# Optimization experiments

Hardware: AMD Instinct MI355X
Metric: run time of the kernel (lower is better)

Reference implementation:

```python
import jax, jax.numpy as jnp
import numpy as np

B, S, D, H, FF = 2, 2048, 1024, 16, 4096
DK = D // H
EPS = 1e-5


def setup_inputs() -> dict:
    key = jax.random.key(0)
    ks = jax.random.split(key, 16)
    sd = 0.02
    return {
        "x": jax.random.normal(ks[0], (B, S, D), jnp.float32),
        "mask": jnp.ones((B, 1, 1, S), jnp.int32),
        "wq_w": jax.random.normal(ks[1], (D, D), jnp.float32) * sd,
        "wq_b": jnp.zeros((D,), jnp.float32),
        "wk_w": jax.random.normal(ks[2], (D, D), jnp.float32) * sd,
        "wk_b": jnp.zeros((D,), jnp.float32),
        "wv_w": jax.random.normal(ks[3], (D, D), jnp.float32) * sd,
        "wv_b": jnp.zeros((D,), jnp.float32),
        "wo_w": jax.random.normal(ks[4], (D, D), jnp.float32) * sd,
        "wo_b": jnp.zeros((D,), jnp.float32),
        "ff1_w": jax.random.normal(ks[5], (FF, D), jnp.float32) * sd,
        "ff1_b": jnp.zeros((FF,), jnp.float32),
        "ff2_w": jax.random.normal(ks[6], (D, FF), jnp.float32) * sd,
        "ff2_b": jnp.zeros((D,), jnp.float32),
        "ln1_a": jnp.ones((D,), jnp.float32),
        "ln1_b": jnp.zeros((D,), jnp.float32),
        "ln2_a": jnp.ones((D,), jnp.float32),
        "ln2_b": jnp.zeros((D,), jnp.float32),
    }


def _layernorm(x, alpha, beta):
    # Matches torch module: std is unbiased (ddof=1), divides by (std + eps)
    mean = jnp.mean(x, -1, keepdims=True)
    std = jnp.std(x, -1, keepdims=True, ddof=1)
    return (x - mean) / (std + EPS) * alpha + beta


def _mha(x, mask, wq_w, wq_b, wk_w, wk_b, wv_w, wv_b, wo_w, wo_b):
    q = (x @ wq_w.T + wq_b).reshape(B, S, H, DK).transpose(0, 2, 1, 3)
    k = (x @ wk_w.T + wk_b).reshape(B, S, H, DK).transpose(0, 2, 1, 3)
    v = (x @ wv_w.T + wv_b).reshape(B, S, H, DK).transpose(0, 2, 1, 3)
    scores = jnp.einsum('bhqd,bhkd->bhqk', q, k) / jnp.sqrt(jnp.float32(DK))
    scores = jnp.where(mask == 0, -jnp.inf, scores)
    attn = jax.nn.softmax(scores, axis=-1)
    out = jnp.einsum('bhqk,bhkd->bhqd', attn, v)
    out = out.transpose(0, 2, 1, 3).reshape(B, S, D)
    return out @ wo_w.T + wo_b


def reference(x, mask, wq_w, wq_b, wk_w, wk_b, wv_w, wv_b, wo_w, wo_b,
              ff1_w, ff1_b, ff2_w, ff2_b, ln1_a, ln1_b, ln2_a, ln2_b):
    # Residual 1: pre-norm + self-attention (dropout = 0)
    h = _layernorm(x, ln1_a, ln1_b)
    x = x + _mha(h, mask, wq_w, wq_b, wk_w, wk_b, wv_w, wv_b, wo_w, wo_b)
    # Residual 2: pre-norm + FFN
    h = _layernorm(x, ln2_a, ln2_b)
    ff = jax.nn.relu(h @ ff1_w.T + ff1_b) @ ff2_w.T + ff2_b
    return x + ff
```

## Files before the change

kernel.cpp:

```cpp
#include <hip/hip_runtime.h>
#include <hip/hip_bf16.h>
#include <stdint.h>

#define B_   2
#define S_   2048
#define D_   1024
#define H_   16
#define FF_  4096
#define TOK  4096
#define EPS_ 1e-5f
#define SC2  0.18033688f

typedef __attribute__((ext_vector_type(8))) short short8;
typedef __attribute__((ext_vector_type(4))) short short4_t;
typedef __attribute__((ext_vector_type(4))) float float4_t;

__device__ __forceinline__ short f2bf(float f) {
  union { float f; uint32_t u; } v; v.f = f;
  uint32_t r = v.u + 0x7fffu + ((v.u >> 16) & 1u);
  return (short)(r >> 16);
}

__device__ __forceinline__ uint32_t pkbf(float a, float b) {
  __hip_bfloat162 h = __float22bfloat162_rn(make_float2(a, b));
  union { __hip_bfloat162 h; uint32_t u; } c; c.h = h; return c.u;
}

__device__ __forceinline__ void gload_lds16(const void* g, void* l) {
  __builtin_amdgcn_global_load_lds(
      (const __attribute__((address_space(1))) void*)g,
      (__attribute__((address_space(3))) void*)l, 16, 0, 0);
}

__global__ void cvt_all(const float* __restrict__ wq, const float* __restrict__ wk,
                        const float* __restrict__ wv, const float* __restrict__ wo,
                        const float* __restrict__ f1, const float* __restrict__ f2,
                        short* __restrict__ out) {
  const int n4 = (12 << 20) / 4;
  int idx = blockIdx.x * blockDim.x + threadIdx.x;
  int stride = gridDim.x * blockDim.x;
  for (int j4 = idx; j4 < n4; j4 += stride) {
    const int j = j4 * 4;
    const int seg = j >> 20;
    const float* src; int off;
    if (seg < 4)      { src = (seg == 0) ? wq : (seg == 1) ? wk : (seg == 2) ? wv : wo;
                        off = j & ((1 << 20) - 1); }
    else if (seg < 8) { src = f1; off = j - (4 << 20); }
    else              { src = f2; off = j - (8 << 20); }
    float4_t v = *(const float4_t*)(src + off);
    short4_t o = { f2bf(v[0]), f2bf(v[1]), f2bf(v[2]), f2bf(v[3]) };
    *(short4_t*)(out + j) = o;
  }
}

__global__ void mask_kernel(const int* __restrict__ m, float* __restrict__ o,
                            int* __restrict__ flags) {
  const int i = blockIdx.x * 64 + threadIdx.x;
  const int mv = m[i];
  o[i] = mv ? 0.0f : -1e30f;
  unsigned long long bal = __ballot(mv == 0);
  if (threadIdx.x == 0) flags[blockIdx.x] = (bal != 0ull) ? 1 : 0;
}

__global__ void combine_kernel(const float* __restrict__ x2, const float* __restrict__ p0,
                               float* __restrict__ out, const float* __restrict__ bias, int n) {
  int idx = blockIdx.x * blockDim.x + threadIdx.x;
  int stride = gridDim.x * blockDim.x;
  for (int j = idx * 4; j < n; j += stride * 4) {
    float4_t a = *(const float4_t*)(x2 + j);
    float4_t b = *(const float4_t*)(p0 + j);
    float4_t c = *(const float4_t*)(out + j);
    float4_t bb = *(const float4_t*)(bias + (j & (D_ - 1)));
    float4_t o = { a[0]+b[0]+c[0]+bb[0], a[1]+b[1]+c[1]+bb[1],
                   a[2]+b[2]+c[2]+bb[2], a[3]+b[3]+c[3]+bb[3] };
    *(float4_t*)(out + j) = o;
  }
}

__global__ __launch_bounds__(256) void ln_kernel(
    const float* __restrict__ x, const float* __restrict__ alpha,
    const float* __restrict__ beta, short* __restrict__ out)
{
  const int row = blockIdx.x;
  const int tid = threadIdx.x;
  const float4_t v = *(const float4_t*)(x + (size_t)row * D_ + tid * 4);
  float s  = v[0] + v[1] + v[2] + v[3];
  float ss = v[0]*v[0] + v[1]*v[1] + v[2]*v[2] + v[3]*v[3];
  #pragma unroll
  for (int m = 1; m < 64; m <<= 1) { s += __shfl_xor(s, m); ss += __shfl_xor(ss, m); }
  __shared__ float red[8];
  const int wave = tid >> 6, lane = tid & 63;
  if (lane == 0) { red[wave] = s; red[4 + wave] = ss; }
  __syncthreads();
  s  = red[0] + red[1] + red[2] + red[3];
  ss = red[4] + red[5] + red[6] + red[7];
  const float mean = s * (1.0f / D_);
  float var = (ss - (float)D_ * mean * mean) * (1.0f / (D_ - 1));
  var = fmaxf(var, 0.0f);
  const float inv = 1.0f / (sqrtf(var) + EPS_);
  short4_t o;
  #pragma unroll
  for (int j = 0; j < 4; j++) {
    float a = alpha[tid*4 + j], bb = beta[tid*4 + j];
    o[j] = f2bf((v[j] - mean) * inv * a + bb);
  }
  *(short4_t*)(out + (size_t)row * D_ + tid * 4) = o;
}

template<int EPI, int BN>
__global__ __launch_bounds__(256) void gemm_bt(
    const short* __restrict__ A, const short* __restrict__ Bm,
    void* __restrict__ Cout, void* __restrict__ Cout2,
    const float* __restrict__ bias, const float* __restrict__ res,
    int N, int K, int lda, int ldb)
{
  __shared__ __align__(16) short As[2][128][32];
  __shared__ __align__(16) short Bs[2][BN][32];

  const int tid  = threadIdx.x;
  const int wave = tid >> 6, lane = tid & 63;
  const int l15  = lane & 15, l4 = lane >> 4;

  const int gx = gridDim.x, gy = gridDim.y;
  int bid = (blockIdx.z * gy + blockIdx.y) * gx + blockIdx.x;
  const int q8 = (gx * gy * gridDim.z) >> 3;
  bid = (bid & 7) * q8 + (bid >> 3);
  const int n0 = (bid % gx) * BN;
  const int m0 = ((bid / gx) % gy) * 128;
  const int zi = bid / (gx * gy);
  const int koff = zi * K;

  constexpr int MI = (BN == 128) ? 4 : 2;
  const int rb = (BN == 128) ? (wave >> 1) * 64 : wave * 32;
  const int cb = (BN == 128) ? (wave & 1) * 64 : 0;

  float4_t acc[MI][4] = {};

  const int scol = (lane & 3) * 8;
  const short* gA0 = A + (size_t)(m0 + wave*32 + (lane >> 2)) * lda + koff + scol;
  const short* gA1 = gA0 + (size_t)16 * lda;
  const short* gB0;
  const short* gB1 = nullptr;
  if (BN == 128) {
    gB0 = Bm + (size_t)(n0 + wave*32 + (lane >> 2)) * ldb + koff + scol;
    gB1 = gB0 + (size_t)16 * ldb;
  } else {
    gB0 = Bm + (size_t)(n0 + wave*16 + (lane >> 2)) * ldb + koff + scol;
  }

  gload_lds16(gA0, &As[0][wave*32][0]);
  gload_lds16(gA1, &As[0][wave*32 + 16][0]);
  if (BN == 128) {
    gload_lds16(gB0, &Bs[0][wave*32][0]);
    gload_lds16(gB1, &Bs[0][wave*32 + 16][0]);
  } else {
    gload_lds16(gB0, &Bs[0][wave*16][0]);
  }

  for (int k0 = 0; k0 < K; k0 += 32) {
    const int cur = (k0 >> 5) & 1;
    __syncthreads();
    if (k0 + 32 < K) {
      gload_lds16(gA0 + k0 + 32, &As[cur^1][wave*32][0]);
      gload_lds16(gA1 + k0 + 32, &As[cur^1][wave*32 + 16][0]);
      if (BN == 128) {
        gload_lds16(gB0 + k0 + 32, &Bs[cur^1][wave*32][0]);
        gload_lds16(gB1 + k0 + 32, &Bs[cur^1][wave*32 + 16][0]);
      } else {
        gload_lds16(gB0 + k0 + 32, &Bs[cur^1][wave*16][0]);
      }
    }
    short8 af[MI], bf[4];
    #pragma unroll
    for (int i = 0; i < MI; i++)
      af[i] = *(const short8*)&As[cur][rb + i*16 + l15][l4*8];
    #pragma unroll
    for (int i = 0; i < 4; i++)
      bf[i] = *(const short8*)&Bs[cur][cb + i*16 + l15][l4*8];
    #pragma unroll
    for (int mi = 0; mi < MI; mi++)
      #pragma unroll
      for (int ni = 0; ni < 4; ni++)
        acc[mi][ni] = __builtin_amdgcn_mfma_f32_16x16x32_bf16(af[mi], bf[ni], acc[mi][ni], 0, 0, 0);
  }

  const int crow0 = m0 + rb + l4*4;
  const int ccol0 = n0 + cb + l15;
  float* dstf = (float*)((EPI == 4 && zi == 1) ? Cout2 : Cout);
  #pragma unroll
  for (int mi = 0; mi < MI; mi++) {
    #pragma unroll
    for (int ni = 0; ni < 4; ni++) {
      const int col = ccol0 + ni*16;
      const float bc = (EPI == 4) ? 0.0f : bias[col];
      #pragma unroll
      for (int r = 0; r < 4; r++) {
        const int row = crow0 + mi*16 + r;
        const float v = acc[mi][ni][r];
        if (EPI == 3) {
          ((float*)Cout)[(size_t)row * N + col] =
              res[(size_t)row * N + col] + v + bc;
        } else {
          dstf[(size_t)row * N + col] = v;
        }
      }
    }
  }
}

#define G256_DECLS                                                            \
  const int tid = threadIdx.x;                                                \
  const int w = tid >> 6, lane = tid & 63;                                    \
  const int wm = w >> 2, wn = w & 3;                                          \
  const int l15 = lane & 15, l4 = lane >> 4;                                  \
  const int srow = w*8 + (lane >> 3);                                         \
  const int schk = ((lane & 7) ^ (((lane >> 5) & 1) << 1)) * 8;               \
  const int rswz = (l4 ^ (((l15 >> 2) & 1) << 1)) * 8;                        \
  const int aoff = (wm*128 + l15) * 64 + rswz;                                \
  const int boff = (wn*64  + l15) * 64 + rswz;

#define G256_STG(buf_, koff_) do {                                            \
    short* da = lds + (buf_)*16384 + w*512;                                   \
    short* db = lds + 32768 + (buf_)*16384 + w*512;                           \
    const short* sa = gA + (koff_);                                           \
    const short* sb = gB + (koff_);                                           \
    gload_lds16(sa,             da);                                          \
    gload_lds16(sa +  64*1024,  da + 4096);                                   \
    gload_lds16(sa + 128*1024,  da + 8192);                                   \
    gload_lds16(sa + 192*1024,  da + 12288);                                  \
    gload_lds16(sb,             db);                                          \
    gload_lds16(sb +  64*1024,  db + 4096);                                   \
    gload_lds16(sb + 128*1024,  db + 8192);                                   \
    gload_lds16(sb + 192*1024,  db + 12288);                                  \
  } while (0)

#define G256_LOOP                                                             \
  float4_t acc[8][4] = {};                                                    \
  G256_STG(0, 0);                                                             \
  G256_STG(1, 64);                                                            \
  for (int t = 0; t < 16; ++t) {                                              \
    const int cur = t & 1;                                                    \
    if (t < 15) asm volatile("s_waitcnt vmcnt(8)" ::: "memory");              \
    else        asm volatile("s_waitcnt vmcnt(0)" ::: "memory");              \
    __builtin_amdgcn_s_barrier();                                             \
    __builtin_amdgcn_sched_barrier(0);                                        \
    const short* La = lds + cur*16384 + aoff;                                 \
    const short* Lb = lds + 32768 + cur*16384 + boff;                         \
    short8 af[4][2], bf0[2][2], bf1[2][2];                                    \
    _Pragma("unroll") for (int mf = 0; mf < 4; mf++)                          \
      _Pragma("unroll") for (int ks = 0; ks < 2; ks++)                        \
        af[mf][ks] = *(const short8*)(La + mf*1024 + ks*32);                  \
    _Pragma("unroll") for (int nf = 0; nf < 2; nf++)                          \
      _Pragma("unroll") for (int ks = 0; ks < 2; ks++)                        \
        bf0[nf][ks] = *(const short8*)(Lb + nf*1024 + ks*32);                 \
    _Pragma("unroll") for (int nf = 0; nf < 2; nf++)                          \
      _Pragma("unroll") for (int ks = 0; ks < 2; ks++)                        \
        bf1[nf][ks] = *(const short8*)(Lb + (2+nf)*1024 + ks*32);             \
    __builtin_amdgcn_s_setprio(1);                                            \
    _Pragma("unroll") for (int mf = 0; mf < 4; mf++)                          \
      _Pragma("unroll") for (int nf = 0; nf < 2; nf++)                        \
        _Pragma("unroll") for (int ks = 0; ks < 2; ks++)                      \
          acc[mf][nf] = __builtin_amdgcn_mfma_f32_16x16x32_bf16(              \
              af[mf][ks], bf0[nf][ks], acc[mf][nf], 0, 0, 0);                 \
    __builtin_amdgcn_s_setprio(0);                                            \
    short8 a2[4][2];                                                          \
    _Pragma("unroll") for (int mf = 0; mf < 4; mf++)                          \
      _Pragma("unroll") for (int ks = 0; ks < 2; ks++)                        \
        a2[mf][ks] = *(const short8*)(La + (4+mf)*1024 + ks*32);              \
    __builtin_amdgcn_s_setprio(1);                                            \
    _Pragma("unroll") for (int mf = 0; mf < 4; mf++)                          \
      _Pragma("unroll") for (int nf = 0; nf < 2; nf++)                        \
        _Pragma("unroll") for (int ks = 0; ks < 2; ks++)                      \
          acc[mf][2+nf] = __builtin_amdgcn_mfma_f32_16x16x32_bf16(            \
              af[mf][ks], bf1[nf][ks], acc[mf][2+nf], 0, 0, 0);               \
    _Pragma("unroll") for (int mf = 0; mf < 4; mf++)                          \
      _Pragma("unroll") for (int nf = 0; nf < 2; nf++)                        \
        _Pragma("unroll") for (int ks = 0; ks < 2; ks++)                      \
          acc[4+mf][2+nf] = __builtin_amdgcn_mfma_f32_16x16x32_bf16(          \
              a2[mf][ks], bf1[nf][ks], acc[4+mf][2+nf], 0, 0, 0);             \
    __builtin_amdgcn_s_setprio(0);                                            \
    __builtin_amdgcn_s_barrier();        \
    if (t < 14) G256_STG(cur, (t+2)*64);                                      \
    __builtin_amdgcn_s_setprio(1);                                            \
    _Pragma("unroll") for (int mf = 0; mf < 4; mf++)                          \
      _Pragma("unroll") for (int nf = 0; nf < 2; nf++)                        \
        _Pragma("unroll") for (int ks = 0; ks < 2; ks++)                      \
          acc[4+mf][nf] = __builtin_amdgcn_mfma_f32_16x16x32_bf16(            \
              a2[mf][ks], bf0[nf][ks], acc[4+mf][nf], 0, 0, 0);               \
    __builtin_amdgcn_s_setprio(0);                                            \
  }

__global__ __launch_bounds__(512, 2) void ff1_256(
    const short* __restrict__ A, const short* __restrict__ Bm,
    short* __restrict__ Cout, const float* __restrict__ bias)
{
  __shared__ __align__(16) short lds[65536];
  G256_DECLS
  const int gx = gridDim.x;
  int bid = blockIdx.y * gx + blockIdx.x;
  const int q8 = (gx * gridDim.y) >> 3;
  bid = (bid & 7) * q8 + (bid >> 3);
  const int n0 = (bid % gx) * 256;
  const int m0 = (bid / gx) * 256;
  const short* gA = A  + (size_t)(m0 + srow) * 1024 + schk;
  const short* gB = Bm + (size_t)(n0 + srow) * 1024 + schk;

  G256_LOOP

  #pragma unroll
  for (int mf = 0; mf < 8; mf++) {
    #pragma unroll
    for (int nf = 0; nf < 4; nf++) {
      const int col = n0 + wn*64 + nf*16 + l15;
      const float bc = bias[col];
      #pragma unroll
      for (int r = 0; r < 4; r++) {
        const int row = m0 + wm*128 + mf*16 + l4*4 + r;
        Cout[(size_t)row * FF_ + col] = f2bf(fmaxf(acc[mf][nf][r] + bc, 0.0f));
      }
    }
  }
}

__global__ __launch_bounds__(512, 2) void qkv_256(
    const short* __restrict__ A, const short* __restrict__ Bm,
    short* __restrict__ qkbuf, short* __restrict__ vt,
    const float* __restrict__ qb, const float* __restrict__ kb,
    const float* __restrict__ vb)
{
  __shared__ __align__(16) short lds[65536];
  G256_DECLS
  const int gx = gridDim.x;
  int bid = blockIdx.y * gx + blockIdx.x;
  const int q8 = (gx * gridDim.y) >> 3;
  bid = (bid & 7) * q8 + (bid >> 3);
  const int n0 = (bid % gx) * 256;
  const int m0 = (bid / gx) * 256;
  const short* gA = A  + (size_t)(m0 + srow) * 1024 + schk;
  const short* gB = Bm + (size_t)(n0 + srow) * 1024 + schk;

  G256_LOOP

  const int seg = n0 >> 10;
  if (seg < 2) {
    const float* bb = seg ? kb : qb;
    const float scl = seg ? 1.0f : SC2;
    #pragma unroll
    for (int mf = 0; mf < 8; mf++)
      #pragma unroll
      for (int nf = 0; nf < 4; nf++) {
        const int col = n0 + wn*64 + nf*16 + l15;
        const float bc = bb[col & 1023];
        #pragma unroll
        for (int r = 0; r < 4; r++) {
          const int row = m0 + wm*128 + mf*16 + l4*4 + r;
          qkbuf[(size_t)row * 2048 + col] = f2bf((acc[mf][nf][r] + bc) * scl);
        }
      }
  } else {
    #pragma unroll
    for (int mf = 0; mf < 8; mf++)
      #pragma unroll
      for (int nf = 0; nf < 4; nf++) {
        const int d = n0 + wn*64 + nf*16 + l15 - 2048;
        const float bc = vb[d];
        const int row0 = m0 + wm*128 + mf*16 + l4*4;
        short4_t o = { f2bf(acc[mf][nf][0] + bc), f2bf(acc[mf][nf][1] + bc),
                       f2bf(acc[mf][nf][2] + bc), f2bf(acc[mf][nf][3] + bc) };
        *(short4_t*)&vt[(size_t)d * TOK + row0] = o;
      }
  }
}

__global__ __launch_bounds__(256, 4) void attn_kernel(
    const short* __restrict__ qk, const short* __restrict__ vt,
    const float* __restrict__ maskb, const int* __restrict__ mflags,
    short* __restrict__ out)
{
  int bid = (blockIdx.z * H_ + blockIdx.y) * (S_/64) + blockIdx.x;
  bid = (bid & 7) * ((B_ * H_ * (S_/64)) >> 3) + (bid >> 3);
  const int qt = bid % (S_/64);
  const int h  = (bid / (S_/64)) % H_;
  const int b  = bid / ((S_/64) * H_);

  const int tid = threadIdx.x, wave = tid >> 6, lane = tid & 63;
  const int l15 = lane & 15, l4 = lane >> 4;
  const int q0 = qt * 64 + wave * 16;

  __shared__ __align__(16) short Kt[2][4096];
  __shared__ __align__(16) short Vt[2][4096];

  short8 qa[2];
  #pragma unroll
  for (int kc = 0; kc < 2; kc++)
    qa[kc] = *(const short8*)&qk[(size_t)(b*S_ + q0 + l15) * 2048 + h*64 + kc*32 + l4*8];

  short8 ones;
  #pragma unroll
  for (int i = 0; i < 8; i++) ones[i] = (short)0x3F80;

  float4_t acc[4];
  #pragma unroll
  for (int dg = 0; dg < 4; dg++) acc[dg] = (float4_t){0.f, 0.f, 0.f, 0.f};
  float4_t accl = (float4_t){0.f, 0.f, 0.f, 0.f};
  float m2 = 0.0f;

  const int r8 = lane >> 3;
  const int ch = (lane & 7) ^ ((r8 & 3) | ((wave & 1) << 2));
  const int sbase = wave * 512;

  #pragma unroll
  for (int i = 0; i < 2; i++) {
    const int row = i*32 + wave*8 + r8;
    gload_lds16(qk + (size_t)(b*S_ + row) * 2048 + 1024 + h*64 + ch*8, &Kt[0][sbase + i*2048]);
    gload_lds16(vt + (size_t)(h*64 + row) * TOK + b*S_ + ch*8,         &Vt[0][sbase + i*2048]);
  }

  int krow[4];
  #pragma unroll
  for (int kg = 0; kg < 4; kg++)
    krow[kg] = 32*(kg>>1) + 8*(l15>>2) + 4*(kg&1) + (l15&3);
  const int gq = (l15 & 3) | (((l15 >> 2) & 1) << 2);
  const int gv = (l15 & 3) | (((l15 >> 3) & 1) << 2);

  for (int t = 0; t < S_/64; t++) {
    const int cur = t & 1;
    __syncthreads();
    if (t + 1 < S_/64) {
      const int k1 = (t + 1) * 64;
      #pragma unroll
      for (int i = 0; i < 2; i++) {
        const int row = i*32 + wave*8 + r8;
        gload_lds16(qk + (size_t)(b*S_ + k1 + row) * 2048 + 1024 + h*64 + ch*8, &Kt[cur^1][sbase + i*2048]);
        gload_lds16(vt + (size_t)(h*64 + row) * TOK + b*S_ + k1 + ch*8,         &Vt[cur^1][sbase + i*2048]);
      }
    }
    const short* Kc = &Kt[cur][0];
    const short* Vc = &Vt[cur][0];

    short8 kf[4][2], vf[4][2];
    #pragma unroll
    for (int kg = 0; kg < 4; kg++)
      #pragma unroll
      for (int kc = 0; kc < 2; kc++)
        kf[kg][kc] = *(const short8*)(Kc + krow[kg]*64 + ((l4 + kc*4) ^ gq) * 8);
    #pragma unroll
    for (int dg = 0; dg < 4; dg++)
      #pragma unroll
      for (int pc = 0; pc < 2; pc++)
        vf[dg][pc] = *(const short8*)(Vc + (dg*16 + l15)*64 + ((l4 + pc*4) ^ gv) * 8);

    const float negm2 = -m2;
    float4_t sc[4];
    #pragma unroll
    for (int kg = 0; kg < 4; kg++)
      sc[kg] = (float4_t){negm2, negm2, negm2, negm2};
    __builtin_amdgcn_s_setprio(1);
    #pragma unroll
    for (int kg = 0; kg < 4; kg++)
      #pragma unroll
      for (int kc = 0; kc < 2; kc++)
        sc[kg] = __builtin_amdgcn_mfma_f32_16x16x32_bf16(kf[kg][kc], qa[kc], sc[kg], 0, 0, 0);
    __builtin_amdgcn_s_setprio(0);

    if (mflags[b*(S_/64) + t]) {
      #pragma unroll
      for (int kg = 0; kg < 4; kg++) {
        float4_t mb = *(const float4_t*)&maskb[b*S_ + t*64 + 32*(kg>>1) + 4*(kg&1) + 8*l4];
        #pragma unroll
        for (int r = 0; r < 4; r++) sc[kg][r] += mb[r];
      }
    }

    float pm = fmaxf(fmaxf(sc[0][0], sc[0][1]), sc[0][2]);
    pm = fmaxf(fmaxf(pm, sc[0][3]), sc[1][0]);
    pm = fmaxf(fmaxf(pm, sc[1][1]), sc[1][2]);
    pm = fmaxf(fmaxf(pm, sc[1][3]), sc[2][0]);
    pm = fmaxf(fmaxf(pm, sc[2][1]), sc[2][2]);
    pm = fmaxf(fmaxf(pm, sc[2][3]), sc[3][0]);
    pm = fmaxf(fmaxf(pm, sc[3][1]), sc[3][2]);
    pm = fmaxf(pm, sc[3][3]);
    pm = fmaxf(pm, __shfl_xor(pm, 16));
    pm = fmaxf(pm, __shfl_xor(pm, 32));
    if (__any(pm > 8.0f)) {
      const float shift = fmaxf(pm, 0.0f);
      m2 += shift;
      const float esc = exp2f(-shift);
      #pragma unroll
      for (int r = 0; r < 4; r++) {
        const float er = __shfl(esc, l4*4 + r);
        #pragma unroll
        for (int dg = 0; dg < 4; dg++) acc[dg][r] *= er;
        accl[r] *= er;
      }
      #pragma unroll
      for (int kg = 0; kg < 4; kg++)
        #pragma unroll
        for (int r = 0; r < 4; r++) sc[kg][r] -= shift;
    }
    #pragma unroll
    for (int kg = 0; kg < 4; kg++)
      #pragma unroll
      for (int r = 0; r < 4; r++)
        sc[kg][r] = exp2f(sc[kg][r]);

    union { short8 s8; uint32_t u[4]; } pu[2];
    #pragma unroll
    for (int pc = 0; pc < 2; pc++) {
      pu[pc].u[0] = pkbf(sc[2*pc][0],   sc[2*pc][1]);
      pu[pc].u[1] = pkbf(sc[2*pc][2],   sc[2*pc][3]);
      pu[pc].u[2] = pkbf(sc[2*pc+1][0], sc[2*pc+1][1]);
      pu[pc].u[3] = pkbf(sc[2*pc+1][2], sc[2*pc+1][3]);
    }
    __builtin_amdgcn_s_setprio(1);
    #pragma unroll
    for (int dg = 0; dg < 4; dg++)
      #pragma unroll
      for (int pc = 0; pc < 2; pc++)
        acc[dg] = __builtin_amdgcn_mfma_f32_16x16x32_bf16(pu[pc].s8, vf[dg][pc], acc[dg], 0, 0, 0);
    #pragma unroll
    for (int pc = 0; pc < 2; pc++)
      accl = __builtin_amdgcn_mfma_f32_16x16x32_bf16(pu[pc].s8, ones, accl, 0, 0, 0);
    __builtin_amdgcn_s_setprio(0);
  }

  float linv[4];
  #pragma unroll
  for (int r = 0; r < 4; r++) linv[r] = 1.0f / accl[r];
  #pragma unroll
  for (int dg = 0; dg < 4; dg++)
    #pragma unroll
    for (int r = 0; r < 4; r++)
      out[(size_t)(b*S_ + q0 + l4*4 + r) * D_ + h*64 + dg*16 + l15] =
          f2bf(acc[dg][r] * linv[r]);
}

extern "C" void kernel_launch(void* const* d_in, const int* in_sizes, int n_in,
                              void* d_out, int out_size, void* d_ws, size_t ws_size,
                              hipStream_t stream)
{
  const float* x     = (const float*)d_in[0];
  const int*   mask  = (const int*)d_in[1];
  const float* wq_w  = (const float*)d_in[2];
  const float* wq_b  = (const float*)d_in[3];
  const float* wk_w  = (const float*)d_in[4];
  const float* wk_b  = (const float*)d_in[5];
  const float* wv_w  = (const float*)d_in[6];
  const float* wv_b  = (const float*)d_in[7];
  const float* wo_w  = (const float*)d_in[8];
  const float* wo_b  = (const float*)d_in[9];
  const float* ff1_w = (const float*)d_in[10];
  const float* ff1_b = (const float*)d_in[11];
  const float* ff2_w = (const float*)d_in[12];
  const float* ff2_b = (const float*)d_in[13];
  const float* ln1_a = (const float*)d_in[14];
  const float* ln1_b = (const float*)d_in[15];
  const float* ln2_a = (const float*)d_in[16];
  const float* ln2_b = (const float*)d_in[17];

  uint8_t* ws = (uint8_t*)d_ws;
  const size_t MB = 1024 * 1024;
  short* wqkv  = (short*)(ws + 0);
  short* wob   = (short*)(ws + 6*MB);
  short* ff1b  = (short*)(ws + 8*MB);
  short* ff2b  = (short*)(ws + 16*MB);
  float* maskb = (float*)(ws + 24*MB + 64*1024);
  int*   mflg  = (int*)(ws + 24*MB + 128*1024);
  short* h1    = (short*)(ws + 25*MB);
  short* attno = (short*)(ws + 25*MB);
  short* qkbuf = (short*)(ws + 33*MB);
  short* vt    = (short*)(ws + 49*MB);
  float* x2    = (float*)(ws + 65*MB);
  short* ffa   = (short*)(ws + 33*MB);
  float* p0f   = (float*)(ws + 0);

  cvt_all<<<2048, 256, 0, stream>>>(wq_w, wk_w, wv_w, wo_w, ff1_w, ff2_w, (short*)ws);
  mask_kernel<<<TOK/64, 64, 0, stream>>>(mask, maskb, mflg);
  ln_kernel<<<TOK, 256, 0, stream>>>(x, ln1_a, ln1_b, h1);
  qkv_256<<<dim3(3072/256, TOK/256), 512, 0, stream>>>(
      h1, wqkv, qkbuf, vt, wq_b, wk_b, wv_b);
  attn_kernel<<<dim3(S_/64, H_, B_), 256, 0, stream>>>(qkbuf, vt, maskb, mflg, attno);
  gemm_bt<3,64><<<dim3(1024/64, TOK/128), 256, 0, stream>>>(
      attno, wob, x2, nullptr, wo_b, x, 1024, 1024, 1024, 1024);
  ln_kernel<<<TOK, 256, 0, stream>>>(x2, ln2_a, ln2_b, h1);
  ff1_256<<<dim3(FF_/256, TOK/256), 512, 0, stream>>>(h1, ff1b, ffa, ff1_b);
  gemm_bt<4,128><<<dim3(1024/128, TOK/128, 2), 256, 0, stream>>>(
      ffa, ff2b, p0f, d_out, nullptr, nullptr, 1024, 2048, FF_, FF_);
  combine_kernel<<<2048, 256, 0, stream>>>(x2, p0f, (float*)d_out, ff2_b, TOK * D_);
}
```

Measured before the change: 250.6 us.

## Move FF2 GEMM to 256x256 pipelined kernel with 4-way split-K and bf16 partials

The FF2 projection switches from the generic 128-tile gemm_bt with a 2-way K split to the 256x256 LDS-pipelined GEMM core, now parameterized by leading dimension, with a 4-way K split. Three of the partials are stored as bf16 and one as fp32 into the output buffer. The combine kernel then sums the residual, bias and all four partials. This aims to use the faster tile schedule and fill more CUs, while the narrower bf16 partials reduce the extra memory traffic split-K adds. In exchange it rounds three partials to bf16, which loses accuracy, and the combine pass reads more buffers.

```diff
diff --git a/kernel.cpp b/kernel.cpp
--- a/kernel.cpp
+++ b/kernel.cpp
@@ -19,6 +19,10 @@
   union { float f; uint32_t u; } v; v.f = f;
   uint32_t r = v.u + 0x7fffu + ((v.u >> 16) & 1u);
   return (short)(r >> 16);
+}
+
+__device__ __forceinline__ float bf2f(short s) {
+  union { uint32_t u; float f; } v; v.u = ((uint32_t)(uint16_t)s) << 16; return v.f;
 }
 
 __device__ __forceinline__ uint32_t pkbf(float a, float b) {
@@ -62,17 +66,24 @@
   if (threadIdx.x == 0) flags[blockIdx.x] = (bal != 0ull) ? 1 : 0;
 }
 
-__global__ void combine_kernel(const float* __restrict__ x2, const float* __restrict__ p0,
-                               float* __restrict__ out, const float* __restrict__ bias, int n) {
+__global__ void combine3_kernel(const float* __restrict__ x2,
+                                const short* __restrict__ pA,
+                                const short* __restrict__ pB,
+                                float* __restrict__ out, const float* __restrict__ bias,
+                                int n) {
   int idx = blockIdx.x * blockDim.x + threadIdx.x;
   int stride = gridDim.x * blockDim.x;
   for (int j = idx * 4; j < n; j += stride * 4) {
-    float4_t a = *(const float4_t*)(x2 + j);
-    float4_t b = *(const float4_t*)(p0 + j);
-    float4_t c = *(const float4_t*)(out + j);
+    float4_t a  = *(const float4_t*)(x2 + j);
+    float4_t c  = *(const float4_t*)(out + j);
     float4_t bb = *(const float4_t*)(bias + (j & (D_ - 1)));
-    float4_t o = { a[0]+b[0]+c[0]+bb[0], a[1]+b[1]+c[1]+bb[1],
-                   a[2]+b[2]+c[2]+bb[2], a[3]+b[3]+c[3]+bb[3] };
+    short4_t q0 = *(const short4_t*)(pA + j);
+    short4_t q1 = *(const short4_t*)(pA + (4u << 20) + j);
+    short4_t q2 = *(const short4_t*)(pB + j);
+    float4_t o;
+    #pragma unroll
+    for (int e = 0; e < 4; e++)
+      o[e] = a[e] + c[e] + bb[e] + bf2f(q0[e]) + bf2f(q1[e]) + bf2f(q2[e]);
     *(float4_t*)(out + j) = o;
   }
 }
@@ -186,23 +197,17 @@
 
   const int crow0 = m0 + rb + l4*4;
   const int ccol0 = n0 + cb + l15;
-  float* dstf = (float*)((EPI == 4 && zi == 1) ? Cout2 : Cout);
   #pragma unroll
   for (int mi = 0; mi < MI; mi++) {
     #pragma unroll
     for (int ni = 0; ni < 4; ni++) {
       const int col = ccol0 + ni*16;
-      const float bc = (EPI == 4) ? 0.0f : bias[col];
+      const float bc = bias[col];
       #pragma unroll
       for (int r = 0; r < 4; r++) {
         const int row = crow0 + mi*16 + r;
-        const float v = acc[mi][ni][r];
-        if (EPI == 3) {
-          ((float*)Cout)[(size_t)row * N + col] =
-              res[(size_t)row * N + col] + v + bc;
-        } else {
-          dstf[(size_t)row * N + col] = v;
-        }
+        ((float*)Cout)[(size_t)row * N + col] =
+            res[(size_t)row * N + col] + acc[mi][ni][r] + bc;
       }
     }
   }
@@ -219,25 +224,25 @@
   const int aoff = (wm*128 + l15) * 64 + rswz;                                \
   const int boff = (wn*64  + l15) * 64 + rswz;
 
-#define G256_STG(buf_, koff_) do {                                            \
+#define G256_STG(buf_, koff_, LDA_) do {                                      \
     short* da = lds + (buf_)*16384 + w*512;                                   \
     short* db = lds + 32768 + (buf_)*16384 + w*512;                           \
     const short* sa = gA + (koff_);                                           \
     const short* sb = gB + (koff_);                                           \
-    gload_lds16(sa,             da);                                          \
-    gload_lds16(sa +  64*1024,  da + 4096);                                   \
-    gload_lds16(sa + 128*1024,  da + 8192);                                   \
-    gload_lds16(sa + 192*1024,  da + 12288);                                  \
-    gload_lds16(sb,             db);                                          \
-    gload_lds16(sb +  64*1024,  db + 4096);                                   \
-    gload_lds16(sb + 128*1024,  db + 8192);                                   \
-    gload_lds16(sb + 192*1024,  db + 12288);                                  \
+    gload_lds16(sa,                      da);                                 \
+    gload_lds16(sa +  64*(size_t)(LDA_), da + 4096);                          \
+    gload_lds16(sa + 128*(size_t)(LDA_), da + 8192);                          \
+    gload_lds16(sa + 192*(size_t)(LDA_), da + 12288);                         \
+    gload_lds16(sb,                      db);                                 \
+    gload_lds16(sb +  64*(size_t)(LDA_), db + 4096);                          \
+    gload_lds16(sb + 128*(size_t)(LDA_), db + 8192);                          \
+    gload_lds16(sb + 192*(size_t)(LDA_), db + 12288);                         \
   } while (0)
 
-#define G256_LOOP                                                             \
+#define G256_LOOP(LDA_)                                                       \
   float4_t acc[8][4] = {};                                                    \
-  G256_STG(0, 0);                                                             \
-  G256_STG(1, 64);                                                            \
+  G256_STG(0, 0, LDA_);                                                       \
+  G256_STG(1, 64, LDA_);                                                      \
   for (int t = 0; t < 16; ++t) {                                              \
     const int cur = t & 1;                                                    \
     if (t < 15) asm volatile("s_waitcnt vmcnt(8)" ::: "memory");              \
@@ -280,7 +285,7 @@
               a2[mf][ks], bf1[nf][ks], acc[4+mf][2+nf], 0, 0, 0);             \
     __builtin_amdgcn_s_setprio(0);                                            \
     __builtin_amdgcn_s_barrier();        \
-    if (t < 14) G256_STG(cur, (t+2)*64);                                      \
+    if (t < 14) G256_STG(cur, (t+2)*64, LDA_);                                \
     __builtin_amdgcn_s_setprio(1);                                            \
     _Pragma("unroll") for (int mf = 0; mf < 4; mf++)                          \
       _Pragma("unroll") for (int nf = 0; nf < 2; nf++)                        \
@@ -305,7 +310,7 @@
   const short* gA = A  + (size_t)(m0 + srow) * 1024 + schk;
   const short* gB = Bm + (size_t)(n0 + srow) * 1024 + schk;
 
-  G256_LOOP
+  G256_LOOP(1024)
 
   #pragma unroll
   for (int mf = 0; mf < 8; mf++) {
@@ -339,7 +344,7 @@
   const short* gA = A  + (size_t)(m0 + srow) * 1024 + schk;
   const short* gB = Bm + (size_t)(n0 + srow) * 1024 + schk;
 
-  G256_LOOP
+  G256_LOOP(1024)
 
   const int seg = n0 >> 10;
   if (seg < 2) {
@@ -368,6 +373,52 @@
         short4_t o = { f2bf(acc[mf][nf][0] + bc), f2bf(acc[mf][nf][1] + bc),
                        f2bf(acc[mf][nf][2] + bc), f2bf(acc[mf][nf][3] + bc) };
         *(short4_t*)&vt[(size_t)d * TOK + row0] = o;
+      }
+  }
+}
+
+__global__ __launch_bounds__(512, 2) void ff2_256(
+    const short* __restrict__ A, const short* __restrict__ Bm,
+    short* __restrict__ pA, short* __restrict__ pB, float* __restrict__ dout)
+{
+  __shared__ __align__(16) short lds[65536];
+  G256_DECLS
+  const int gx = gridDim.x, gy = gridDim.y;
+  int bid = (blockIdx.z * gy + blockIdx.y) * gx + blockIdx.x;
+  const int q8 = (gx * gy * gridDim.z) >> 3;
+  bid = (bid & 7) * q8 + (bid >> 3);
+  const int n0 = (bid % gx) * 256;
+  const int m0 = ((bid / gx) % gy) * 256;
+  const int zi = bid / (gx * gy);
+  const short* gA = A  + (size_t)(m0 + srow) * 4096 + zi*1024 + schk;
+  const short* gB = Bm + (size_t)(n0 + srow) * 4096 + zi*1024 + schk;
+
+  G256_LOOP(4096)
+
+  if (zi < 3) {
+    short* dst = (zi < 2) ? (pA + (size_t)zi * (4u << 20)) : pB;
+    #pragma unroll
+    for (int mf = 0; mf < 8; mf++)
+      #pragma unroll
+      for (int nf = 0; nf < 4; nf++) {
+        const int col = n0 + wn*64 + nf*16 + l15;
+        #pragma unroll
+        for (int r = 0; r < 4; r++) {
+          const int row = m0 + wm*128 + mf*16 + l4*4 + r;
+          dst[(size_t)row * D_ + col] = f2bf(acc[mf][nf][r]);
+        }
+      }
+  } else {
+    #pragma unroll
+    for (int mf = 0; mf < 8; mf++)
+      #pragma unroll
+      for (int nf = 0; nf < 4; nf++) {
+        const int col = n0 + wn*64 + nf*16 + l15;
+        #pragma unroll
+        for (int r = 0; r < 4; r++) {
+          const int row = m0 + wm*128 + mf*16 + l4*4 + r;
+          dout[(size_t)row * D_ + col] = acc[mf][nf][r];
+        }
       }
   }
 }
@@ -568,11 +619,12 @@
   int*   mflg  = (int*)(ws + 24*MB + 128*1024);
   short* h1    = (short*)(ws + 25*MB);
   short* attno = (short*)(ws + 25*MB);
+  short* pB    = (short*)(ws + 25*MB);
   short* qkbuf = (short*)(ws + 33*MB);
   short* vt    = (short*)(ws + 49*MB);
   float* x2    = (float*)(ws + 65*MB);
   short* ffa   = (short*)(ws + 33*MB);
-  float* p0f   = (float*)(ws + 0);
+  short* pA    = (short*)(ws + 0);
 
   cvt_all<<<2048, 256, 0, stream>>>(wq_w, wk_w, wv_w, wo_w, ff1_w, ff2_w, (short*)ws);
   mask_kernel<<<TOK/64, 64, 0, stream>>>(mask, maskb, mflg);
@@ -584,7 +636,7 @@
       attno, wob, x2, nullptr, wo_b, x, 1024, 1024, 1024, 1024);
   ln_kernel<<<TOK, 256, 0, stream>>>(x2, ln2_a, ln2_b, h1);
   ff1_256<<<dim3(FF_/256, TOK/256), 512, 0, stream>>>(h1, ff1b, ffa, ff1_b);
-  gemm_bt<4,128><<<dim3(1024/128, TOK/128, 2), 256, 0, stream>>>(
-      ffa, ff2b, p0f, d_out, nullptr, nullptr, 1024, 2048, FF_, FF_);
-  combine_kernel<<<2048, 256, 0, stream>>>(x2, p0f, (float*)d_out, ff2_b, TOK * D_);
-}
+  ff2_256<<<dim3(1024/256, TOK/256, 4), 512, 0, stream>>>(
+      ffa, ff2b, pA, pB, (float*)d_out);
+  combine3_kernel<<<2048, 256, 0, stream>>>(x2, pA, pB, (float*)d_out, ff2_b, TOK * D_);
+}
```

Result: faster. 243.4 us (-2.9%).
